# Kernel tuning notes

Hardware: AMD Instinct MI355X
Metric: run time of the kernel (lower is better)

The kernel has to match this reference:

```python
import jax, jax.numpy as jnp
import numpy as np

B, R, C, NH, G = 32, 64, 96, 3, 8   # batch, patches_resolution, dim, heads, group(window) size
HD = C // NH                         # head dim = 32
SCALE = HD ** -0.5
HID = 4 * C                          # mlp hidden = mlp_ratio * dim


def setup_inputs() -> dict:
    key = jax.random.key(0)
    ks = jax.random.split(key, 16)
    n = jax.random.normal
    s = 0.02
    return {
        "x": n(ks[0], (B, R * R, C), jnp.float32),
        "w_qkv": n(ks[1], (C, 3 * C), jnp.float32) * s,
        "b_qkv": jnp.zeros((3 * C,), jnp.float32),
        "w_lepe": n(ks[2], (C, 1, 3, 3), jnp.float32) * s,  # depthwise conv, OIHW with groups=C
        "b_lepe": jnp.zeros((C,), jnp.float32),
        "w_proj": n(ks[3], (C, C), jnp.float32) * s,
        "b_proj": jnp.zeros((C,), jnp.float32),
        "g1": jnp.ones((C,), jnp.float32),
        "bt1": jnp.zeros((C,), jnp.float32),
        "g2": jnp.ones((C,), jnp.float32),
        "bt2": jnp.zeros((C,), jnp.float32),
        "w_fc1": n(ks[4], (C, HID), jnp.float32) * s,
        "b_fc1": jnp.zeros((HID,), jnp.float32),
        "w_fc2": n(ks[5], (HID, C), jnp.float32) * s,
        "b_fc2": jnp.zeros((C,), jnp.float32),
    }


def _ln(x, g, b):
    m = x.mean(-1, keepdims=True)
    v = ((x - m) ** 2).mean(-1, keepdims=True)
    return (x - m) * jax.lax.rsqrt(v + 1e-5) * g + b


def reference(x, w_qkv, b_qkv, w_lepe, b_lepe, w_proj, b_proj,
              g1, bt1, g2, bt2, w_fc1, b_fc1, w_fc2, b_fc2):
    Bn, L, _ = x.shape
    H = W = R
    shortcut = x
    # norm1 + SDA window partition: (B,H,W,C) -> (B*nW, G*G, C)
    h = _ln(x, g1, bt1).reshape(Bn, H // G, G, W // G, G, C)
    h = h.transpose(0, 1, 3, 2, 4, 5).reshape(-1, G * G, C)
    B_ = h.shape[0]
    qkv = (h @ w_qkv + b_qkv).reshape(B_, G * G, 3, NH, HD).transpose(2, 0, 3, 1, 4)
    q, k, v = qkv[0], qkv[1], qkv[2]            # (B_, NH, G*G, HD)
    # LePE: depthwise 3x3 conv on V viewed as (B_, C, G, G)
    vimg = v.transpose(0, 1, 3, 2).reshape(B_, C, G, G)
    lepe = jax.lax.conv_general_dilated(
        vimg, w_lepe, window_strides=(1, 1), padding='SAME',
        feature_group_count=C, dimension_numbers=('NCHW', 'OIHW', 'NCHW'))
    lepe = lepe + b_lepe[None, :, None, None]
    lepe = lepe.reshape(B_, NH, HD, G * G).transpose(0, 1, 3, 2)  # (B_, NH, G*G, HD)
    # attention (no mask registered in this block)
    attn = jax.nn.softmax((q * SCALE) @ k.transpose(0, 1, 3, 2), axis=-1)
    o = (attn @ v + lepe).transpose(0, 2, 1, 3).reshape(B_, G * G, C)
    o = o @ w_proj + b_proj
    # window reverse
    o = o.reshape(Bn, H // G, W // G, G, G, C).transpose(0, 1, 3, 2, 4, 5).reshape(Bn, L, C)
    x1 = shortcut + o
    # MLP block (exact GELU, as torch nn.GELU default)
    m = _ln(x1, g2, bt2)
    m = jax.nn.gelu(m @ w_fc1 + b_fc1, approximate=False) @ w_fc2 + b_fc2
    return (x1 + m, attn)
```

## Files before the change

### kernel.cpp

```cpp
#include <hip/hip_runtime.h>
#include <hip/hip_bf16.h>

typedef short short8 __attribute__((ext_vector_type(8)));
typedef float f32x4 __attribute__((ext_vector_type(4)));

constexpr int BDIM = 32, RDIM = 64, CDIM = 96, NH_ = 3, HD_ = 32;
constexpr int LTOK = RDIM * RDIM;
constexpr int GG = 64;
constexpr int HID = 384;
constexpr int NWIN = 2048;
constexpr float SCALE = 0.17677669529663687f;
constexpr long OUT1OFF = (long)BDIM * LTOK * CDIM;

constexpr int O_WQKVT = 0;
constexpr int O_WPROJT = 27648;
constexpr int O_WFC1T = 36864;
constexpr int O_WFC2T = 73728;
constexpr int W_TOT = 110592;

__device__ __forceinline__ unsigned short f2b(float f) {
  return __builtin_bit_cast(unsigned short, __float2bfloat16(f));
}
__device__ __forceinline__ float b2f(unsigned short u) {
  return __bfloat162float(__builtin_bit_cast(__hip_bfloat16, u));
}

__device__ __forceinline__ float gelu_f(float x) {
  float u = x * 0.70710678118654752f;
  float ax = __builtin_fabsf(u);
  float t = __builtin_amdgcn_rcpf(1.f + 0.3275911f * ax);
  float poly = t * (0.254829592f +
               t * (-0.284496736f +
               t * (1.421413741f +
               t * (-1.453152027f +
               t * 1.061405429f))));
  float erf_abs = 1.f - poly * __expf(-ax * ax);
  float erf_u = (u < 0.f) ? -erf_abs : erf_abs;
  return 0.5f * x * (1.f + erf_u);
}

__global__ void prep_weights(const float* __restrict__ wqkv,
                             const float* __restrict__ wproj,
                             const float* __restrict__ wfc1,
                             const float* __restrict__ wfc2,
                             unsigned short* __restrict__ ws) {
  int i = blockIdx.x * 256 + threadIdx.x;
  if (i >= W_TOT) return;
  float v;
  if (i < O_WPROJT) {
    int n = i / 96, k = i - n * 96;
    v = wqkv[k * 288 + n];
  } else if (i < O_WFC1T) {
    int j = i - O_WPROJT, n = j / 96, k = j - n * 96;
    v = wproj[k * 96 + n];
  } else if (i < O_WFC2T) {
    int j = i - O_WFC1T, n = j / 96, k = j - n * 96;
    v = wfc1[k * 384 + n];
  } else {
    int j = i - O_WFC2T, n = j / 384, k = j - n * 384;
    v = wfc2[k * 96 + n];
  }
  ws[i] = f2b(v);
}

__global__ __launch_bounds__(256, 2)
void attn_mfma(const float* __restrict__ x, const float* __restrict__ bqkv,
               const float* __restrict__ wlepe, const float* __restrict__ blepe,
               const float* __restrict__ bproj, const float* __restrict__ g1,
               const float* __restrict__ bt1,
               const unsigned short* __restrict__ ws, float* __restrict__ out) {
  constexpr int SA = 104;
  constexpr int SQ = 200;
  constexpr int SV = 72;
  constexpr int SP = 72;
  __shared__ __attribute__((aligned(16))) unsigned short hA[64 * SA];
  __shared__ __attribute__((aligned(16))) unsigned short qkS[64 * SQ];
  __shared__ __attribute__((aligned(16))) unsigned short vS[96 * SV];
  __shared__ __attribute__((aligned(16))) unsigned short pS[64 * SP];
  float* red = (float*)pS;

  const int tid = threadIdx.x, lane = tid & 63;
  const int wv = __builtin_amdgcn_readfirstlane(tid >> 6);
  const int w = blockIdx.x, b = w >> 6, wi = w & 63, wr = wi >> 3, wc = wi & 7;
  const long xbase = (long)b * (LTOK * CDIM);
  const int l15 = lane & 15, lk = (lane >> 4) * 8, lr = (lane >> 4) * 4;

  {
    const int tok = lane;
    const long rowbase =
        xbase + (long)((wr * 8 + (tok >> 3)) * RDIM + wc * 8 + (tok & 7)) * CDIM;
    float xv[24], s1 = 0.f, s2 = 0.f;
#pragma unroll
    for (int i = 0; i < 24; ++i) {
      float v = x[rowbase + wv * 24 + i];
      xv[i] = v; s1 += v; s2 += v * v;
    }
    red[wv * 64 + tok] = s1;
    red[256 + wv * 64 + tok] = s2;
    __syncthreads();
    float m = 0.f, vv = 0.f;
#pragma unroll
    for (int q = 0; q < 4; ++q) { m += red[q * 64 + tok]; vv += red[256 + q * 64 + tok]; }
    m *= (1.f / 96.f);
    vv = vv * (1.f / 96.f) - m * m;
    float rs = rsqrtf(vv + 1e-5f);
#pragma unroll
    for (int i = 0; i < 24; ++i) {
      int c = wv * 24 + i;
      hA[tok * SA + c] = f2b((xv[i] - m) * rs * g1[c] + bt1[c]);
    }
  }
  __syncthreads();

  {
    f32x4 acc[18];
#pragma unroll
    for (int t = 0; t < 18; ++t) acc[t] = (f32x4){0.f, 0.f, 0.f, 0.f};
    const int arow = wv * 16 + l15;
#pragma unroll
    for (int kk = 0; kk < 3; ++kk) {
      short8 a = *(const short8*)&hA[arow * SA + kk * 32 + lk];
#pragma unroll
      for (int nt = 0; nt < 18; ++nt) {
        short8 bw = *(const short8*)&ws[O_WQKVT + (nt * 16 + l15) * 96 + kk * 32 + lk];
        acc[nt] = __builtin_amdgcn_mfma_f32_16x16x32_bf16(a, bw, acc[nt], 0, 0, 0);
      }
    }
#pragma unroll
    for (int nt = 0; nt < 18; ++nt) {
      int n0 = nt * 16 + l15;
      float bias = bqkv[n0];
#pragma unroll
      for (int r = 0; r < 4; ++r) {
        int tk = wv * 16 + lr + r;
        float v = acc[nt][r] + bias;
        if (n0 < 96) qkS[tk * SQ + n0] = f2b(v * SCALE);
        else if (n0 < 192) qkS[tk * SQ + n0] = f2b(v);
        else vS[(n0 - 192) * SV + tk] = f2b(v);
      }
    }
  }
  __syncthreads();

  for (int h = 0; h < NH_; ++h) {
    f32x4 sacc[4];
#pragma unroll
    for (int t = 0; t < 4; ++t) sacc[t] = (f32x4){0.f, 0.f, 0.f, 0.f};
    short8 aq = *(const short8*)&qkS[(wv * 16 + l15) * SQ + h * 32 + lk];
#pragma unroll
    for (int nt = 0; nt < 4; ++nt) {
      short8 bk = *(const short8*)&qkS[(nt * 16 + l15) * SQ + 96 + h * 32 + lk];
      sacc[nt] = __builtin_amdgcn_mfma_f32_16x16x32_bf16(aq, bk, sacc[nt], 0, 0, 0);
    }
    float p[4][4];
#pragma unroll
    for (int r = 0; r < 4; ++r) {
      float mx = -1e30f;
#pragma unroll
      for (int nt = 0; nt < 4; ++nt) mx = fmaxf(mx, sacc[nt][r]);
#pragma unroll
      for (int s = 1; s < 16; s <<= 1) mx = fmaxf(mx, __shfl_xor(mx, s, 64));
      float sum = 0.f;
#pragma unroll
      for (int nt = 0; nt < 4; ++nt) {
        float e = __expf(sacc[nt][r] - mx);
        p[nt][r] = e; sum += e;
      }
#pragma unroll
      for (int s = 1; s < 16; s <<= 1) sum += __shfl_xor(sum, s, 64);
      float inv = 1.f / sum;
#pragma unroll
      for (int nt = 0; nt < 4; ++nt) p[nt][r] *= inv;
    }
    const long o1base = OUT1OFF + ((long)(w * NH_ + h) * GG) * GG;
#pragma unroll
    for (int nt = 0; nt < 4; ++nt) {
      int col = nt * 16 + l15;
#pragma unroll
      for (int r = 0; r < 4; ++r) {
        int row = wv * 16 + lr + r;
        out[o1base + (long)row * GG + col] = p[nt][r];
        pS[row * SP + col] = f2b(p[nt][r]);
      }
    }
    f32x4 oa[2];
    oa[0] = (f32x4){0.f, 0.f, 0.f, 0.f};
    oa[1] = (f32x4){0.f, 0.f, 0.f, 0.f};
#pragma unroll
    for (int kk = 0; kk < 2; ++kk) {
      short8 ap = *(const short8*)&pS[(wv * 16 + l15) * SP + kk * 32 + lk];
#pragma unroll
      for (int nt = 0; nt < 2; ++nt) {
        short8 bv = *(const short8*)&vS[(h * 32 + nt * 16 + l15) * SV + kk * 32 + lk];
        oa[nt] = __builtin_amdgcn_mfma_f32_16x16x32_bf16(ap, bv, oa[nt], 0, 0, 0);
      }
    }
#pragma unroll
    for (int nt = 0; nt < 2; ++nt) {
      int d = nt * 16 + l15, c = h * 32 + d;
      float lw9[9];
#pragma unroll
      for (int q = 0; q < 9; ++q) lw9[q] = wlepe[c * 9 + q];
      float lb = blepe[c];
#pragma unroll
      for (int r = 0; r < 4; ++r) {
        int tk = wv * 16 + lr + r;
        int tr_ = tk >> 3, tc_ = tk & 7;
        float a = lb;
#pragma unroll
        for (int kh = 0; kh < 3; ++kh)
#pragma unroll
          for (int kw2 = 0; kw2 < 3; ++kw2) {
            int rr = tr_ + kh - 1, cc = tc_ + kw2 - 1;
            if (rr >= 0 && rr < 8 && cc >= 0 && cc < 8)
              a += lw9[kh * 3 + kw2] * b2f(vS[c * SV + rr * 8 + cc]);
          }
        hA[tk * SA + c] = f2b(oa[nt][r] + a);
      }
    }
  }
  __syncthreads();

  {
    f32x4 pacc[6];
#pragma unroll
    for (int t = 0; t < 6; ++t) pacc[t] = (f32x4){0.f, 0.f, 0.f, 0.f};
#pragma unroll
    for (int kk = 0; kk < 3; ++kk) {
      short8 ao = *(const short8*)&hA[(wv * 16 + l15) * SA + kk * 32 + lk];
#pragma unroll
      for (int nt = 0; nt < 6; ++nt) {
        short8 bw = *(const short8*)&ws[O_WPROJT + (nt * 16 + l15) * 96 + kk * 32 + lk];
        pacc[nt] = __builtin_amdgcn_mfma_f32_16x16x32_bf16(ao, bw, pacc[nt], 0, 0, 0);
      }
    }
#pragma unroll
    for (int nt = 0; nt < 6; ++nt) {
      int ch = nt * 16 + l15;
      float bias = bproj[ch];
#pragma unroll
      for (int r = 0; r < 4; ++r) {
        int tk = wv * 16 + lr + r;
        long g = xbase + (long)((wr * 8 + (tk >> 3)) * RDIM + wc * 8 + (tk & 7)) * CDIM + ch;
        out[g] = x[g] + pacc[nt][r] + bias;
      }
    }
  }
}

__global__ __launch_bounds__(256, 4)
void mlp_mfma(const float* __restrict__ bfc1, const float* __restrict__ bfc2,
              const float* __restrict__ g2, const float* __restrict__ bt2,
              const unsigned short* __restrict__ ws, float* __restrict__ out) {
  constexpr int SB = 104;
  constexpr int SHQ = 104;
  __shared__ __attribute__((aligned(16))) unsigned short hB[64 * SB];
  __shared__ __attribute__((aligned(16))) unsigned short Hq[64 * SHQ];

  const int tid = threadIdx.x, lane = tid & 63;
  const int wv = __builtin_amdgcn_readfirstlane(tid >> 6);
  const long t0 = (long)blockIdx.x * GG;
  const int l15 = lane & 15, lk = (lane >> 4) * 8, lr = (lane >> 4) * 4;
  const int p = lane >> 4;
  const int tok = wv * 16 + l15;

  {
    const float* rb = out + (t0 + tok) * CDIM + p * 24;
    float xv[24], s1 = 0.f, s2 = 0.f;
#pragma unroll
    for (int i = 0; i < 6; ++i) {
      f32x4 v4 = *(const f32x4*)(rb + i * 4);
#pragma unroll
      for (int j = 0; j < 4; ++j) {
        float v = v4[j];
        xv[i * 4 + j] = v; s1 += v; s2 += v * v;
      }
    }
    s1 += __shfl_xor(s1, 16, 64); s1 += __shfl_xor(s1, 32, 64);
    s2 += __shfl_xor(s2, 16, 64); s2 += __shfl_xor(s2, 32, 64);
    float m = s1 * (1.f / 96.f);
    float vv = s2 * (1.f / 96.f) - m * m;
    float rs = rsqrtf(vv + 1e-5f);
    unsigned short tmp[24];
#pragma unroll
    for (int i = 0; i < 24; ++i) {
      int c = p * 24 + i;
      tmp[i] = f2b((xv[i] - m) * rs * g2[c] + bt2[c]);
    }
#pragma unroll
    for (int i = 0; i < 3; ++i)
      *(short8*)&hB[tok * SB + p * 24 + i * 8] = *(const short8*)&tmp[i * 8];
  }

  f32x4 acc2[6];
#pragma unroll
  for (int t = 0; t < 6; ++t) acc2[t] = (f32x4){0.f, 0.f, 0.f, 0.f};

#pragma unroll 1
  for (int q = 0; q < 4; ++q) {
    f32x4 acc1[6];
#pragma unroll
    for (int t = 0; t < 6; ++t) acc1[t] = (f32x4){0.f, 0.f, 0.f, 0.f};
#pragma unroll
    for (int kk = 0; kk < 3; ++kk) {
      short8 a = *(const short8*)&hB[(wv * 16 + l15) * SB + kk * 32 + lk];
#pragma unroll
      for (int nt = 0; nt < 6; ++nt) {
        int n = q * 96 + nt * 16 + l15;
        short8 bw = *(const short8*)&ws[O_WFC1T + n * 96 + kk * 32 + lk];
        acc1[nt] = __builtin_amdgcn_mfma_f32_16x16x32_bf16(a, bw, acc1[nt], 0, 0, 0);
      }
    }
#pragma unroll
    for (int nt = 0; nt < 6; ++nt) {
      int n = q * 96 + nt * 16 + l15;
      float bias = bfc1[n];
#pragma unroll
      for (int r = 0; r < 4; ++r) {
        int tk = wv * 16 + lr + r;
        Hq[tk * SHQ + nt * 16 + l15] = f2b(gelu_f(acc1[nt][r] + bias));
      }
    }
#pragma unroll
    for (int kk = 0; kk < 3; ++kk) {
      short8 a = *(const short8*)&Hq[(wv * 16 + l15) * SHQ + kk * 32 + lk];
#pragma unroll
      for (int nt = 0; nt < 6; ++nt) {
        short8 bw = *(const short8*)&ws[O_WFC2T + (nt * 16 + l15) * 384 + q * 96 + kk * 32 + lk];
        acc2[nt] = __builtin_amdgcn_mfma_f32_16x16x32_bf16(a, bw, acc2[nt], 0, 0, 0);
      }
    }
  }

#pragma unroll
  for (int nt = 0; nt < 6; ++nt) {
    int ch = nt * 16 + l15;
    float bias = bfc2[ch];
#pragma unroll
    for (int r = 0; r < 4; ++r) {
      int tk = wv * 16 + lr + r;
      long g = (t0 + tk) * CDIM + ch;
      out[g] = out[g] + acc2[nt][r] + bias;
    }
  }
}

struct PF {
  const float *x, *w_qkv, *b_qkv, *w_lepe, *b_lepe, *w_proj, *b_proj;
  const float *g1, *bt1, *g2, *bt2, *w_fc1, *b_fc1, *w_fc2, *b_fc2;
  float* out;
};

__global__ __launch_bounds__(256, 2)
void attn_scalar(PF p) {
  constexpr int SA = 66;
  __shared__ __hip_bfloat16 bufA[CDIM * SA];
  __shared__ __hip_bfloat16 qkvT[288 * GG];
  __shared__ __hip_bfloat16 sPad[GG * SA];
  __shared__ float meanS[GG], rstdS[GG];

  const int w = blockIdx.x;
  const int b = w >> 6, wi = w & 63, wr = wi >> 3, wc = wi & 7;
  const int tid = threadIdx.x, lane = tid & 63;
  const int wv = __builtin_amdgcn_readfirstlane(tid >> 6);
  const long xbase = (long)b * (LTOK * CDIM);

  for (int k = 0; k < 24; ++k) {
    int e = tid + k * 256, wrow = e / 768, o = e - wrow * 768;
    int tir = o / 96, ch = o - tir * 96;
    long g = xbase + ((wr * 8 + wrow) * RDIM + wc * 8 + tir) * CDIM + ch;
    bufA[ch * SA + wrow * 8 + tir] = __float2bfloat16(p.x[g]);
  }
  __syncthreads();
  if (wv == 0) {
    float m = 0.f;
    for (int c = 0; c < CDIM; ++c) m += __bfloat162float(bufA[c * SA + lane]);
    m *= (1.f / CDIM);
    float var = 0.f;
    for (int c = 0; c < CDIM; ++c) {
      float d = __bfloat162float(bufA[c * SA + lane]) - m;
      var += d * d;
    }
    meanS[lane] = m;
    rstdS[lane] = rsqrtf(var * (1.f / CDIM) + 1e-5f);
  }
  __syncthreads();
  {
    float m = meanS[lane], rs = rstdS[lane];
    for (int cc = 0; cc < 24; ++cc) {
      int c = wv * 24 + cc;
      float v = __bfloat162float(bufA[c * SA + lane]);
      bufA[c * SA + lane] = __float2bfloat16((v - m) * rs * p.g1[c] + p.bt1[c]);
    }
  }
  __syncthreads();
  for (int tile = 0; tile < 2; ++tile) {
    int j0 = wv * 72 + tile * 36;
    float acc[36];
#pragma unroll
    for (int jj = 0; jj < 36; ++jj) acc[jj] = p.b_qkv[j0 + jj];
#pragma unroll 1
    for (int c = 0; c < CDIM; ++c) {
      float hv = __bfloat162float(bufA[c * SA + lane]);
#pragma unroll
      for (int jj = 0; jj < 36; ++jj) acc[jj] += hv * p.w_qkv[c * 288 + j0 + jj];
    }
#pragma unroll
    for (int jj = 0; jj < 36; ++jj)
      qkvT[(j0 + jj) * GG + lane] = __float2bfloat16(acc[jj]);
  }
  __syncthreads();
  for (int hh = 0; hh < NH_; ++hh) {
    float kreg[HD_];
#pragma unroll
    for (int d = 0; d < HD_; ++d)
      kreg[d] = __bfloat162float(qkvT[(CDIM + hh * HD_ + d) * GG + lane]);
#pragma unroll 1
    for (int r = 0; r < 16; ++r) {
      int i = wv * 16 + r;
      float acc = 0.f;
#pragma unroll
      for (int d = 0; d < HD_; ++d)
        acc += __bfloat162float(qkvT[(hh * HD_ + d) * GG + i]) * kreg[d];
      sPad[lane * SA + i] = __float2bfloat16(acc * SCALE);
    }
#pragma unroll 1
    for (int r = 0; r < 16; ++r) {
      int i = wv * 16 + r;
      float v = __bfloat162float(sPad[lane * SA + i]);
      float mx = v;
#pragma unroll
      for (int s = 32; s > 0; s >>= 1) mx = fmaxf(mx, __shfl_xor(mx, s, 64));
      float e = __expf(v - mx);
      float sum = e;
#pragma unroll
      for (int s = 32; s > 0; s >>= 1) sum += __shfl_xor(sum, s, 64);
      float rr = e / sum;
      sPad[lane * SA + i] = __float2bfloat16(rr);
      p.out[OUT1OFF + ((long)(w * NH_ + hh) * GG + i) * GG + lane] = rr;
    }
    __syncthreads();
    {
      int d0 = wv * 8;
      float acc[8];
#pragma unroll
      for (int dd = 0; dd < 8; ++dd) acc[dd] = 0.f;
#pragma unroll 1
      for (int j = 0; j < GG; ++j) {
        float sv = __bfloat162float(sPad[j * SA + lane]);
#pragma unroll
        for (int dd = 0; dd < 8; ++dd)
          acc[dd] += sv * __bfloat162float(qkvT[(2 * CDIM + hh * HD_ + d0 + dd) * GG + j]);
      }
      int tr = lane >> 3, tc = lane & 7;
#pragma unroll
      for (int dd = 0; dd < 8; ++dd) {
        int c = hh * HD_ + d0 + dd;
        float a = p.b_lepe[c];
#pragma unroll
        for (int kh = 0; kh < 3; ++kh)
#pragma unroll
          for (int kw = 0; kw < 3; ++kw) {
            int rr2 = tr + kh - 1, cc2 = tc + kw - 1;
            if (rr2 >= 0 && rr2 < 8 && cc2 >= 0 && cc2 < 8)
              a += p.w_lepe[c * 9 + kh * 3 + kw] *
                   __bfloat162float(qkvT[(2 * CDIM + hh * HD_ + d0 + dd) * GG + rr2 * 8 + cc2]);
          }
        acc[dd] += a;
      }
#pragma unroll
      for (int dd = 0; dd < 8; ++dd)
        bufA[(hh * HD_ + d0 + dd) * SA + lane] = __float2bfloat16(acc[dd]);
    }
    __syncthreads();
  }
  __hip_bfloat16* projT = qkvT;
  {
    int j0 = wv * 24;
    float acc[24];
#pragma unroll
    for (int jj = 0; jj < 24; ++jj) acc[jj] = p.b_proj[j0 + jj];
#pragma unroll 1
    for (int c = 0; c < CDIM; ++c) {
      float ov = __bfloat162float(bufA[c * SA + lane]);
#pragma unroll
      for (int jj = 0; jj < 24; ++jj) acc[jj] += ov * p.w_proj[c * CDIM + j0 + jj];
    }
#pragma unroll
    for (int jj = 0; jj < 24; ++jj)
      projT[(j0 + jj) * SA + lane] = __float2bfloat16(acc[jj]);
  }
  __syncthreads();
  for (int k = 0; k < 24; ++k) {
    int e = tid + k * 256, wrow = e / 768, o = e - wrow * 768;
    int tir = o / 96, ch = o - tir * 96;
    long g = xbase + ((wr * 8 + wrow) * RDIM + wc * 8 + tir) * CDIM + ch;
    p.out[g] = p.x[g] + __bfloat162float(projT[ch * SA + wrow * 8 + tir]);
  }
}

__global__ __launch_bounds__(256, 2)
void mlp_scalar(PF p) {
  constexpr int SB = 66;
  __shared__ __hip_bfloat16 bufB[CDIM * SB];
  __shared__ __hip_bfloat16 hidT[HID * GG];
  __shared__ float meanS[GG], rstdS[GG];

  const int tid = threadIdx.x, lane = tid & 63;
  const int wv = __builtin_amdgcn_readfirstlane(tid >> 6);
  const long t0 = (long)blockIdx.x * GG;

  for (int k = 0; k < 24; ++k) {
    int e = tid + k * 256, tok = e / 96, ch = e - tok * 96;
    bufB[ch * SB + tok] = __float2bfloat16(p.out[(t0 + tok) * CDIM + ch]);
  }
  __syncthreads();
  if (wv == 0) {
    float m = 0.f;
    for (int c = 0; c < CDIM; ++c) m += __bfloat162float(bufB[c * SB + lane]);
    m *= (1.f / CDIM);
    float var = 0.f;
    for (int c = 0; c < CDIM; ++c) {
      float d = __bfloat162float(bufB[c * SB + lane]) - m;
      var += d * d;
    }
    meanS[lane] = m;
    rstdS[lane] = rsqrtf(var * (1.f / CDIM) + 1e-5f);
  }
  __syncthreads();
  {
    float m = meanS[lane], rs = rstdS[lane];
    for (int cc = 0; cc < 24; ++cc) {
      int c = wv * 24 + cc;
      float v = __bfloat162float(bufB[c * SB + lane]);
      bufB[c * SB + lane] = __float2bfloat16((v - m) * rs * p.g2[c] + p.bt2[c]);
    }
  }
  __syncthreads();
  for (int tile = 0; tile < 4; ++tile) {
    int j0 = wv * 96 + tile * 24;
    float acc[24];
#pragma unroll
    for (int jj = 0; jj < 24; ++jj) acc[jj] = p.b_fc1[j0 + jj];
#pragma unroll 1
    for (int c = 0; c < CDIM; ++c) {
      float hv = __bfloat162float(bufB[c * SB + lane]);
#pragma unroll
      for (int jj = 0; jj < 24; ++jj) acc[jj] += hv * p.w_fc1[c * HID + j0 + jj];
    }
#pragma unroll
    for (int jj = 0; jj < 24; ++jj) {
      float xg = acc[jj];
      hidT[(j0 + jj) * GG + lane] =
          __float2bfloat16(0.5f * xg * (1.f + erff(xg * 0.70710678118f)));
    }
  }
  __syncthreads();
  {
    int j0 = wv * 24;
    float acc[24];
#pragma unroll
    for (int jj = 0; jj < 24; ++jj) acc[jj] = p.b_fc2[j0 + jj];
#pragma unroll 1
    for (int h = 0; h < HID; ++h) {
      float hv = __bfloat162float(hidT[h * GG + lane]);
#pragma unroll
      for (int jj = 0; jj < 24; ++jj) acc[jj] += hv * p.w_fc2[h * CDIM + j0 + jj];
    }
#pragma unroll
    for (int jj = 0; jj < 24; ++jj)
      bufB[(j0 + jj) * SB + lane] = __float2bfloat16(acc[jj]);
  }
  __syncthreads();
  for (int k = 0; k < 24; ++k) {
    int e = tid + k * 256, tok = e / 96, ch = e - tok * 96;
    long g = (t0 + tok) * CDIM + ch;
    p.out[g] = p.out[g] + __bfloat162float(bufB[ch * SB + tok]);
  }
}

extern "C" void kernel_launch(void* const* d_in, const int* in_sizes, int n_in,
                              void* d_out, int out_size, void* d_ws, size_t ws_size,
                              hipStream_t stream) {
  const float* x = (const float*)d_in[0];
  const float* w_qkv = (const float*)d_in[1];
  const float* b_qkv = (const float*)d_in[2];
  const float* w_lepe = (const float*)d_in[3];
  const float* b_lepe = (const float*)d_in[4];
  const float* w_proj = (const float*)d_in[5];
  const float* b_proj = (const float*)d_in[6];
  const float* g1 = (const float*)d_in[7];
  const float* bt1 = (const float*)d_in[8];
  const float* g2 = (const float*)d_in[9];
  const float* bt2 = (const float*)d_in[10];
  const float* w_fc1 = (const float*)d_in[11];
  const float* b_fc1 = (const float*)d_in[12];
  const float* w_fc2 = (const float*)d_in[13];
  const float* b_fc2 = (const float*)d_in[14];
  float* out = (float*)d_out;
  const int mlp_blocks = (BDIM * LTOK) / GG;

  if (ws_size >= (size_t)W_TOT * sizeof(unsigned short)) {
    unsigned short* ws = (unsigned short*)d_ws;
    prep_weights<<<(W_TOT + 255) / 256, 256, 0, stream>>>(w_qkv, w_proj, w_fc1, w_fc2, ws);
    attn_mfma<<<NWIN, 256, 0, stream>>>(x, b_qkv, w_lepe, b_lepe, b_proj, g1, bt1, ws, out);
    mlp_mfma<<<mlp_blocks, 256, 0, stream>>>(b_fc1, b_fc2, g2, bt2, ws, out);
  } else {
    PF p{x, w_qkv, b_qkv, w_lepe, b_lepe, w_proj, b_proj,
         g1, bt1, g2, bt2, w_fc1, b_fc1, w_fc2, b_fc2, out};
    attn_scalar<<<NWIN, 256, 0, stream>>>(p);
    mlp_scalar<<<mlp_blocks, 256, 0, stream>>>(p);
  }
}
```

Baseline: 405.5 us.

## Restructure attention LayerNorm and LePE to cut block barriers and redundant conv work

LayerNorm is reorganized so each wave normalizes its own 16 tokens. Four lanes per token share the work, partial sums are combined with lane shuffles, and loads and stores use vector widths, which removes a shared-memory reduction and a block barrier. The depthwise LePE convolution moves into a dedicated pass after the QKV GEMM: each thread buffers V rows in registers, computes without per-tap bounds checks, and writes into hA. The head loop then only adds the attention output, and the barrier before the projection is dropped. MFMA loops are wrapped in s_setprio to favor matrix issue, at the cost of an extra barrier and higher register pressure in the LePE pass.

```diff
diff --git a/kernel.cpp b/kernel.cpp
--- a/kernel.cpp
+++ b/kernel.cpp
@@ -77,46 +77,54 @@
   __shared__ __attribute__((aligned(16))) unsigned short qkS[64 * SQ];
   __shared__ __attribute__((aligned(16))) unsigned short vS[96 * SV];
   __shared__ __attribute__((aligned(16))) unsigned short pS[64 * SP];
-  float* red = (float*)pS;
 
   const int tid = threadIdx.x, lane = tid & 63;
   const int wv = __builtin_amdgcn_readfirstlane(tid >> 6);
   const int w = blockIdx.x, b = w >> 6, wi = w & 63, wr = wi >> 3, wc = wi & 7;
   const long xbase = (long)b * (LTOK * CDIM);
   const int l15 = lane & 15, lk = (lane >> 4) * 8, lr = (lane >> 4) * 4;
-
-  {
-    const int tok = lane;
+  const int p = lane >> 4;
+  const int tok = wv * 16 + l15;
+
+  {
     const long rowbase =
         xbase + (long)((wr * 8 + (tok >> 3)) * RDIM + wc * 8 + (tok & 7)) * CDIM;
+    const float* rb = x + rowbase + p * 24;
     float xv[24], s1 = 0.f, s2 = 0.f;
 #pragma unroll
-    for (int i = 0; i < 24; ++i) {
-      float v = x[rowbase + wv * 24 + i];
-      xv[i] = v; s1 += v; s2 += v * v;
-    }
-    red[wv * 64 + tok] = s1;
-    red[256 + wv * 64 + tok] = s2;
-    __syncthreads();
-    float m = 0.f, vv = 0.f;
-#pragma unroll
-    for (int q = 0; q < 4; ++q) { m += red[q * 64 + tok]; vv += red[256 + q * 64 + tok]; }
-    m *= (1.f / 96.f);
-    vv = vv * (1.f / 96.f) - m * m;
+    for (int i = 0; i < 6; ++i) {
+      f32x4 v4 = *(const f32x4*)(rb + i * 4);
+#pragma unroll
+      for (int j = 0; j < 4; ++j) {
+        float v = v4[j];
+        xv[i * 4 + j] = v; s1 += v; s2 += v * v;
+      }
+    }
+    s1 += __shfl_xor(s1, 16, 64); s1 += __shfl_xor(s1, 32, 64);
+    s2 += __shfl_xor(s2, 16, 64); s2 += __shfl_xor(s2, 32, 64);
+    float m = s1 * (1.f / 96.f);
+    float vv = s2 * (1.f / 96.f) - m * m;
     float rs = rsqrtf(vv + 1e-5f);
-#pragma unroll
-    for (int i = 0; i < 24; ++i) {
-      int c = wv * 24 + i;
-      hA[tok * SA + c] = f2b((xv[i] - m) * rs * g1[c] + bt1[c]);
-    }
-  }
-  __syncthreads();
+    unsigned short tmp[24];
+#pragma unroll
+    for (int i = 0; i < 6; ++i) {
+      f32x4 gv = *(const f32x4*)(g1 + p * 24 + i * 4);
+      f32x4 bv = *(const f32x4*)(bt1 + p * 24 + i * 4);
+#pragma unroll
+      for (int j = 0; j < 4; ++j)
+        tmp[i * 4 + j] = f2b((xv[i * 4 + j] - m) * rs * gv[j] + bv[j]);
+    }
+#pragma unroll
+    for (int i = 0; i < 3; ++i)
+      *(short8*)&hA[tok * SA + p * 24 + i * 8] = *(const short8*)&tmp[i * 8];
+  }
 
   {
     f32x4 acc[18];
 #pragma unroll
     for (int t = 0; t < 18; ++t) acc[t] = (f32x4){0.f, 0.f, 0.f, 0.f};
     const int arow = wv * 16 + l15;
+    __builtin_amdgcn_s_setprio(1);
 #pragma unroll
     for (int kk = 0; kk < 3; ++kk) {
       short8 a = *(const short8*)&hA[arow * SA + kk * 32 + lk];
@@ -126,6 +134,7 @@
         acc[nt] = __builtin_amdgcn_mfma_f32_16x16x32_bf16(a, bw, acc[nt], 0, 0, 0);
       }
     }
+    __builtin_amdgcn_s_setprio(0);
 #pragma unroll
     for (int nt = 0; nt < 18; ++nt) {
       int n0 = nt * 16 + l15;
@@ -142,6 +151,45 @@
   }
   __syncthreads();
 
+  if (tid < 192) {
+    const int c = tid >> 1;
+    const int half = tid & 1;
+    const int r0 = half * 4;
+    float rowb[6][8];
+#pragma unroll
+    for (int rr = 0; rr < 6; ++rr) {
+      int vr = r0 - 1 + rr;
+      if (vr >= 0 && vr < 8) {
+        short8 v8 = *(const short8*)&vS[c * SV + vr * 8];
+#pragma unroll
+        for (int j = 0; j < 8; ++j) rowb[rr][j] = b2f((unsigned short)v8[j]);
+      } else {
+#pragma unroll
+        for (int j = 0; j < 8; ++j) rowb[rr][j] = 0.f;
+      }
+    }
+    float lw9[9];
+#pragma unroll
+    for (int q = 0; q < 9; ++q) lw9[q] = wlepe[c * 9 + q];
+    const float lb = blepe[c];
+#pragma unroll
+    for (int r = 0; r < 4; ++r) {
+#pragma unroll
+      for (int cc = 0; cc < 8; ++cc) {
+        float a = lb;
+#pragma unroll
+        for (int kh = 0; kh < 3; ++kh) {
+          const float* rbp = rowb[r + kh];
+          if (cc > 0) a += lw9[kh * 3 + 0] * rbp[cc - 1];
+          a += lw9[kh * 3 + 1] * rbp[cc];
+          if (cc < 7) a += lw9[kh * 3 + 2] * rbp[cc + 1];
+        }
+        hA[((r0 + r) * 8 + cc) * SA + c] = f2b(a);
+      }
+    }
+  }
+  __syncthreads();
+
   for (int h = 0; h < NH_; ++h) {
     f32x4 sacc[4];
 #pragma unroll
@@ -152,7 +200,7 @@
       short8 bk = *(const short8*)&qkS[(nt * 16 + l15) * SQ + 96 + h * 32 + lk];
       sacc[nt] = __builtin_amdgcn_mfma_f32_16x16x32_bf16(aq, bk, sacc[nt], 0, 0, 0);
     }
-    float p[4][4];
+    float pr[4][4];
 #pragma unroll
     for (int r = 0; r < 4; ++r) {
       float mx = -1e30f;
@@ -164,13 +212,13 @@
 #pragma unroll
       for (int nt = 0; nt < 4; ++nt) {
         float e = __expf(sacc[nt][r] - mx);
-        p[nt][r] = e; sum += e;
+        pr[nt][r] = e; sum += e;
       }
 #pragma unroll
       for (int s = 1; s < 16; s <<= 1) sum += __shfl_xor(sum, s, 64);
       float inv = 1.f / sum;
 #pragma unroll
-      for (int nt = 0; nt < 4; ++nt) p[nt][r] *= inv;
+      for (int nt = 0; nt < 4; ++nt) pr[nt][r] *= inv;
     }
     const long o1base = OUT1OFF + ((long)(w * NH_ + h) * GG) * GG;
 #pragma unroll
@@ -179,8 +227,8 @@
 #pragma unroll
       for (int r = 0; r < 4; ++r) {
         int row = wv * 16 + lr + r;
-        out[o1base + (long)row * GG + col] = p[nt][r];
-        pS[row * SP + col] = f2b(p[nt][r]);
+        out[o1base + (long)row * GG + col] = pr[nt][r];
+        pS[row * SP + col] = f2b(pr[nt][r]);
       }
     }
     f32x4 oa[2];
@@ -197,34 +245,20 @@
     }
 #pragma unroll
     for (int nt = 0; nt < 2; ++nt) {
-      int d = nt * 16 + l15, c = h * 32 + d;
-      float lw9[9];
-#pragma unroll
-      for (int q = 0; q < 9; ++q) lw9[q] = wlepe[c * 9 + q];
-      float lb = blepe[c];
+      int c = h * 32 + nt * 16 + l15;
 #pragma unroll
       for (int r = 0; r < 4; ++r) {
         int tk = wv * 16 + lr + r;
-        int tr_ = tk >> 3, tc_ = tk & 7;
-        float a = lb;
-#pragma unroll
-        for (int kh = 0; kh < 3; ++kh)
-#pragma unroll
-          for (int kw2 = 0; kw2 < 3; ++kw2) {
-            int rr = tr_ + kh - 1, cc = tc_ + kw2 - 1;
-            if (rr >= 0 && rr < 8 && cc >= 0 && cc < 8)
-              a += lw9[kh * 3 + kw2] * b2f(vS[c * SV + rr * 8 + cc]);
-          }
-        hA[tk * SA + c] = f2b(oa[nt][r] + a);
-      }
-    }
-  }
-  __syncthreads();
+        hA[tk * SA + c] = f2b(oa[nt][r] + b2f(hA[tk * SA + c]));
+      }
+    }
+  }
 
   {
     f32x4 pacc[6];
 #pragma unroll
     for (int t = 0; t < 6; ++t) pacc[t] = (f32x4){0.f, 0.f, 0.f, 0.f};
+    __builtin_amdgcn_s_setprio(1);
 #pragma unroll
     for (int kk = 0; kk < 3; ++kk) {
       short8 ao = *(const short8*)&hA[(wv * 16 + l15) * SA + kk * 32 + lk];
@@ -234,6 +268,7 @@
         pacc[nt] = __builtin_amdgcn_mfma_f32_16x16x32_bf16(ao, bw, pacc[nt], 0, 0, 0);
       }
     }
+    __builtin_amdgcn_s_setprio(0);
 #pragma unroll
     for (int nt = 0; nt < 6; ++nt) {
       int ch = nt * 16 + l15;
```

Result: faster. 377.3 us (-7.0%).
